# Kernel tuning notes

Hardware: AMD Instinct MI355X
Metric: run time of the kernel (lower is better)

Reference implementation:

```python
import jax, jax.numpy as jnp
import numpy as np

NEG_BIG = -9e15
ALPHA = 0.1  # leaky relu slope


def setup_inputs() -> dict:
    key = jax.random.key(0)
    k1, k2, k3, k4 = jax.random.split(key, 4)
    B, C, N, F = 4, 4, 2048, 64
    x = jax.random.normal(k1, (B, C, N, F), dtype=jnp.float32)
    adj = jax.random.randint(k2, (N, N), 0, 2, dtype=jnp.int32)
    # xavier_uniform on shape (1,1,F,1): fan_in=1, fan_out=F -> bound = 1.414*sqrt(6/(1+F))
    bound = 1.414 * np.sqrt(6.0 / (1.0 + F))
    a1 = jax.random.uniform(k3, (F, 1), jnp.float32, -bound, bound)
    a2 = jax.random.uniform(k4, (F, 1), jnp.float32, -bound, bound)
    return {"x": x, "adj": adj, "a1": a1, "a2": a2}


def reference(x, adj, a1, a2):
    # x: [B, C, N, F]; adj: [N, N]; a1, a2: [F, 1]
    h = x
    f1 = jnp.einsum("bcnf,fo->bcn", h, a1)  # [B, C, N]
    f2 = jnp.einsum("bcnf,fo->bcn", h, a2)  # [B, C, N]
    e = f1[..., :, None] + f2[..., None, :]  # [B, C, N, N] additive scores
    e = jnp.where(e > 0, e, ALPHA * e)       # leaky relu
    e = jnp.where(adj[None, None] > 0, e, jnp.float32(NEG_BIG))
    attention = jax.nn.softmax(e, axis=-1)
    # dropout is identity in eval mode (training=False)
    return jnp.matmul(attention, h)          # [B, C, N, F]
```

## Files before the change

kernel.cpp:

```cpp
#include <hip/hip_runtime.h>
#include <hip/hip_bf16.h>
#include <cstdint>

#define NN 2048
#define FF 64
#define BCC 16

typedef float f32x4 __attribute__((ext_vector_type(4)));
typedef _Float16 half8 __attribute__((ext_vector_type(8)));
typedef uint32_t u32x4 __attribute__((ext_vector_type(4)));


__global__ __launch_bounds__(256) void k_prep(const float* __restrict__ x,
        const int* __restrict__ adj,
        const float* __restrict__ a1, const float* __restrict__ a2,
        _Float16* __restrict__ xP, _Float16* __restrict__ Uh,
        _Float16* __restrict__ Vh, _Float16* __restrict__ CIh,
        unsigned char* __restrict__ ADJP) {
    int wid  = threadIdx.x >> 6;
    int lane = threadIdx.x & 63;

    if (blockIdx.x >= 512) {
        int idx = (blockIdx.x - 512) * 4 + wid;
        int row = idx >> 3, cg = idx & 7;
        const int* p = adj + (size_t)row * NN + cg * 256 + lane;
        unsigned long long m0 = __ballot(p[0]   > 0);
        unsigned long long m1 = __ballot(p[64]  > 0);
        unsigned long long m2 = __ballot(p[128] > 0);
        unsigned long long m3 = __ballot(p[192] > 0);
        if (lane < 32) {
            int q = lane >> 3, s = lane & 7;
            unsigned long long m = (q == 0) ? m0 : (q == 1) ? m1
                                 : (q == 2) ? m2 : m3;
            unsigned char byte = (unsigned char)(m >> (8 * s));
            int jt = (cg * 4 + q) * 2 + (s >> 2);
            int g  = s & 3;
            ADJP[(size_t)row * 256 + g * 64 + jt] = byte;
        }
        return;
    }

    __shared__ float tile[64][65];
    __shared__ float red[2][64][4];
    int bc = blockIdx.x >> 5;
    int n0 = (blockIdx.x & 31) * 64;
    int tx = lane;
    int ty = wid;
    const float* xp = x + ((size_t)bc * NN + n0) * FF;
    #pragma unroll
    for (int k = 0; k < 16; k++) {
        int nl = ty * 16 + k;
        tile[nl][tx] = xp[(size_t)nl * FF + tx];
    }
    __syncthreads();
    int g = lane >> 4, l15 = lane & 15;
    int jt0 = n0 >> 5;
    #pragma unroll
    for (int jl = 0; jl < 2; jl++) {
        half8 val;
        #pragma unroll
        for (int e = 0; e < 8; e++)
            val[e] = (_Float16)tile[jl * 32 + 8 * g + e][ty * 16 + l15];
        ((half8*)xP)[(((size_t)bc * 64 + jt0 + jl) * 4 + ty) * 64 + lane] = val;
    }
    float d1 = 0.f, d2 = 0.f;
    #pragma unroll
    for (int i = 0; i < 16; i++) {
        int f = ty * 16 + i;
        float xv = tile[tx][f];
        d1 += xv * a1[f];
        d2 += xv * a2[f];
    }
    red[0][tx][ty] = d1;
    red[1][tx][ty] = d2;
    __syncthreads();
    if (ty == 0) {
        float f1 = red[0][tx][0] + red[0][tx][1] + red[0][tx][2] + red[0][tx][3];
        float f2 = red[1][tx][0] + red[1][tx][1] + red[1][tx][2] + red[1][tx][3];
        int idx = bc * NN + n0 + tx;
        Uh[idx]  = (_Float16)expf(f2);
        Vh[idx]  = (_Float16)expf(0.1f * f2);
        CIh[idx] = (_Float16)expf(-0.9f * f1);
    }
}

__global__ __launch_bounds__(256) void k_main(
        const _Float16* __restrict__ xP, const _Float16* __restrict__ Uh,
        const _Float16* __restrict__ Vh, const _Float16* __restrict__ CIh,
        const unsigned char* __restrict__ ADJP, float* __restrict__ out) {
    __shared__ _Float16 su[2048];
    __shared__ _Float16 sv[2048];
    __shared__ u32x4 lut[256];
    __shared__ float part[4][16][68];
    __shared__ float zp[4][16];

    int tid = threadIdx.x;
    int jq = tid >> 6, lane = tid & 63;
    int l15 = lane & 15, g = lane >> 4;

    int xcd = blockIdx.x & 7, kk = blockIdx.x >> 3;
    int bc   = (xcd << 1) | (kk >> 5);
    int iblk = kk & 31;
    int i0   = iblk * 64;

    ((u32x4*)su)[tid] = ((const u32x4*)(Uh + bc * NN))[tid];
    ((u32x4*)sv)[tid] = ((const u32x4*)(Vh + bc * NN))[tid];
    {
        uint32_t bb = tid;
        u32x4 lv;
        #pragma unroll
        for (int w = 0; w < 4; w++)
            lv[w] = (((bb >> (2 * w)) & 1u) ? 0xFFFFu : 0u)
                  | (((bb >> (2 * w + 1)) & 1u) ? 0xFFFF0000u : 0u);
        lut[bb] = lv;
    }
    const unsigned char* ab = ADJP + g * 64 + jq * 16;
    u32x4 adjw0 = *(const u32x4*)(ab + (size_t)(i0 + l15) * 256);
    u32x4 adjw1 = *(const u32x4*)(ab + (size_t)(i0 + 16 + l15) * 256);
    u32x4 adjw2 = *(const u32x4*)(ab + (size_t)(i0 + 32 + l15) * 256);
    u32x4 adjw3 = *(const u32x4*)(ab + (size_t)(i0 + 48 + l15) * 256);
    _Float16 Ci0 = CIh[bc * NN + i0 + l15];
    _Float16 Ci1 = CIh[bc * NN + i0 + 16 + l15];
    _Float16 Ci2 = CIh[bc * NN + i0 + 32 + l15];
    _Float16 Ci3 = CIh[bc * NN + i0 + 48 + l15];
    __syncthreads();

    f32x4 acc[4][4];
    #pragma unroll
    for (int a = 0; a < 4; a++)
        #pragma unroll
        for (int nb = 0; nb < 4; nb++)
            acc[a][nb] = (f32x4){0.f, 0.f, 0.f, 0.f};
    f32x4 accz[4];
    #pragma unroll
    for (int a = 0; a < 4; a++) accz[a] = (f32x4){0.f, 0.f, 0.f, 0.f};
    half8 onesh;
    #pragma unroll
    for (int e = 0; e < 8; e++) onesh[e] = (_Float16)1.0f;

    const u32x4* xPbc = (const u32x4*)xP + (size_t)bc * 16384;

    u32x4 A_x0, A_x1, A_x2, A_x3, B_x0, B_x1, B_x2, B_x3;

#define LOADX(P, J) do {                                                      \
        const u32x4* xw_ = xPbc + (((size_t)(jq * 16 + (J))) << 8) + lane;    \
        P##x0 = xw_[0]; P##x1 = xw_[64]; P##x2 = xw_[128]; P##x3 = xw_[192];  \
    } while (0)

#define GEN(AF, ADJW, CI) do {                                                \
        uint32_t b_ = (ADJW[(J_) >> 2] >> (((J_) & 3) * 8)) & 0xffu;          \
        u32x4 mm_ = lut[b_];                                                  \
        half8 mx_ = __builtin_elementwise_max(uu_, vv_ * (CI));               \
        AF = __builtin_bit_cast(half8, __builtin_bit_cast(u32x4, mx_) & mm_); \
    } while (0)

#define COMP(P, J) do {                                                       \
        const int J_ = (J);                                                   \
        const int jo_ = (jq * 16 + J_) * 32 + 8 * g;                          \
        half8 uu_ = *(const half8*)&su[jo_];                                  \
        half8 vv_ = *(const half8*)&sv[jo_];                                  \
        half8 af0_, af1_, af2_, af3_;                                         \
        GEN(af0_, adjw0, Ci0); GEN(af1_, adjw1, Ci1);                         \
        GEN(af2_, adjw2, Ci2); GEN(af3_, adjw3, Ci3);                         \
        half8 b0_ = __builtin_bit_cast(half8, P##x0);                         \
        half8 b1_ = __builtin_bit_cast(half8, P##x1);                         \
        half8 b2_ = __builtin_bit_cast(half8, P##x2);                         \
        half8 b3_ = __builtin_bit_cast(half8, P##x3);                         \
        acc[0][0] = __builtin_amdgcn_mfma_f32_16x16x32_f16(af0_, b0_, acc[0][0], 0, 0, 0); \
        acc[0][1] = __builtin_amdgcn_mfma_f32_16x16x32_f16(af0_, b1_, acc[0][1], 0, 0, 0); \
        acc[0][2] = __builtin_amdgcn_mfma_f32_16x16x32_f16(af0_, b2_, acc[0][2], 0, 0, 0); \
        acc[0][3] = __builtin_amdgcn_mfma_f32_16x16x32_f16(af0_, b3_, acc[0][3], 0, 0, 0); \
        accz[0]   = __builtin_amdgcn_mfma_f32_16x16x32_f16(af0_, onesh, accz[0], 0, 0, 0); \
        acc[1][0] = __builtin_amdgcn_mfma_f32_16x16x32_f16(af1_, b0_, acc[1][0], 0, 0, 0); \
        acc[1][1] = __builtin_amdgcn_mfma_f32_16x16x32_f16(af1_, b1_, acc[1][1], 0, 0, 0); \
        acc[1][2] = __builtin_amdgcn_mfma_f32_16x16x32_f16(af1_, b2_, acc[1][2], 0, 0, 0); \
        acc[1][3] = __builtin_amdgcn_mfma_f32_16x16x32_f16(af1_, b3_, acc[1][3], 0, 0, 0); \
        accz[1]   = __builtin_amdgcn_mfma_f32_16x16x32_f16(af1_, onesh, accz[1], 0, 0, 0); \
        acc[2][0] = __builtin_amdgcn_mfma_f32_16x16x32_f16(af2_, b0_, acc[2][0], 0, 0, 0); \
        acc[2][1] = __builtin_amdgcn_mfma_f32_16x16x32_f16(af2_, b1_, acc[2][1], 0, 0, 0); \
        acc[2][2] = __builtin_amdgcn_mfma_f32_16x16x32_f16(af2_, b2_, acc[2][2], 0, 0, 0); \
        acc[2][3] = __builtin_amdgcn_mfma_f32_16x16x32_f16(af2_, b3_, acc[2][3], 0, 0, 0); \
        accz[2]   = __builtin_amdgcn_mfma_f32_16x16x32_f16(af2_, onesh, accz[2], 0, 0, 0); \
        acc[3][0] = __builtin_amdgcn_mfma_f32_16x16x32_f16(af3_, b0_, acc[3][0], 0, 0, 0); \
        acc[3][1] = __builtin_amdgcn_mfma_f32_16x16x32_f16(af3_, b1_, acc[3][1], 0, 0, 0); \
        acc[3][2] = __builtin_amdgcn_mfma_f32_16x16x32_f16(af3_, b2_, acc[3][2], 0, 0, 0); \
        acc[3][3] = __builtin_amdgcn_mfma_f32_16x16x32_f16(af3_, b3_, acc[3][3], 0, 0, 0); \
        accz[3]   = __builtin_amdgcn_mfma_f32_16x16x32_f16(af3_, onesh, accz[3], 0, 0, 0); \
    } while (0)

    LOADX(A_, 0);
    LOADX(B_, 1);  COMP(A_, 0);
    LOADX(A_, 2);  COMP(B_, 1);
    LOADX(B_, 3);  COMP(A_, 2);
    LOADX(A_, 4);  COMP(B_, 3);
    LOADX(B_, 5);  COMP(A_, 4);
    LOADX(A_, 6);  COMP(B_, 5);
    LOADX(B_, 7);  COMP(A_, 6);
    LOADX(A_, 8);  COMP(B_, 7);
    LOADX(B_, 9);  COMP(A_, 8);
    LOADX(A_, 10); COMP(B_, 9);
    LOADX(B_, 11); COMP(A_, 10);
    LOADX(A_, 12); COMP(B_, 11);
    LOADX(B_, 13); COMP(A_, 12);
    LOADX(A_, 14); COMP(B_, 13);
    LOADX(B_, 15); COMP(A_, 14);
    COMP(B_, 15);
#undef LOADX
#undef GEN
#undef COMP

    float* outp = out + ((size_t)bc * NN + i0) * FF;
    #pragma unroll
    for (int a = 0; a < 4; a++) {
        #pragma unroll
        for (int nb = 0; nb < 4; nb++)
            #pragma unroll
            for (int r = 0; r < 4; r++)
                part[jq][4 * g + r][nb * 16 + l15] = acc[a][nb][r];
        if (l15 == 0) {
            #pragma unroll
            for (int r = 0; r < 4; r++)
                zp[jq][4 * g + r] = accz[a][r];
        }
        __syncthreads();
        #pragma unroll
        for (int rr = 0; rr < 4; rr++) {
            int row = jq * 4 + rr;
            float s = part[0][row][lane] + part[1][row][lane]
                    + part[2][row][lane] + part[3][row][lane];
            float z = zp[0][row] + zp[1][row] + zp[2][row] + zp[3][row];
            outp[(size_t)(16 * a + row) * FF + lane] = s / z;
        }
        __syncthreads();
    }
}

extern "C" void kernel_launch(void* const* d_in, const int* in_sizes, int n_in,
                              void* d_out, int out_size, void* d_ws, size_t ws_size,
                              hipStream_t stream) {
    const float* x  = (const float*)d_in[0];
    const int* adj  = (const int*)d_in[1];
    const float* a1 = (const float*)d_in[2];
    const float* a2 = (const float*)d_in[3];
    float* out = (float*)d_out;

    char* ws = (char*)d_ws;
    _Float16* xP  = (_Float16*)ws;
    _Float16* Uh  = (_Float16*)(ws + 4194304);
    _Float16* Vh  = (_Float16*)(ws + 4259840);
    _Float16* CIh = (_Float16*)(ws + 4325376);
    unsigned char* ADJP = (unsigned char*)(ws + 4390912);

    k_prep<<<512 + 4096, 256, 0, stream>>>(x, adj, a1, a2, xP, Uh, Vh, CIh, ADJP);
    k_main<<<512, 256, 0, stream>>>(xP, Uh, Vh, CIh, ADJP, out);
}
```

Before: 26.36 us.

## Use 512-thread blocks covering 128 rows, sharing U/V staging across two row groups

Result: slower. 26.92 us (+2.1%).

```diff
diff --git a/kernel.cpp b/kernel.cpp
--- a/kernel.cpp
+++ b/kernel.cpp
@@ -84,45 +84,49 @@
     }
 }
 
-__global__ __launch_bounds__(256) void k_main(
+union SmemU {
+    struct { _Float16 su[2048]; _Float16 sv[2048]; u32x4 lut[256]; } s;
+    struct { float part[8][16][68]; float zp[8][16]; } e;
+};
+
+__global__ __launch_bounds__(512, 2) void k_main(
         const _Float16* __restrict__ xP, const _Float16* __restrict__ Uh,
         const _Float16* __restrict__ Vh, const _Float16* __restrict__ CIh,
         const unsigned char* __restrict__ ADJP, float* __restrict__ out) {
-    __shared__ _Float16 su[2048];
-    __shared__ _Float16 sv[2048];
-    __shared__ u32x4 lut[256];
-    __shared__ float part[4][16][68];
-    __shared__ float zp[4][16];
+    __shared__ SmemU sm;
 
     int tid = threadIdx.x;
-    int jq = tid >> 6, lane = tid & 63;
+    int wid = tid >> 6, lane = tid & 63;
+    int ig = wid >> 2, jq = wid & 3;
     int l15 = lane & 15, g = lane >> 4;
 
     int xcd = blockIdx.x & 7, kk = blockIdx.x >> 3;
-    int bc   = (xcd << 1) | (kk >> 5);
-    int iblk = kk & 31;
-    int i0   = iblk * 64;
-
-    ((u32x4*)su)[tid] = ((const u32x4*)(Uh + bc * NN))[tid];
-    ((u32x4*)sv)[tid] = ((const u32x4*)(Vh + bc * NN))[tid];
-    {
+    int bc   = (xcd << 1) | (kk >> 4);
+    int iblk = kk & 15;
+    int i0   = iblk * 128;
+    int rb   = i0 + ig * 64;
+
+    if (tid < 256) {
+        ((u32x4*)sm.s.su)[tid] = ((const u32x4*)(Uh + bc * NN))[tid];
         uint32_t bb = tid;
         u32x4 lv;
         #pragma unroll
         for (int w = 0; w < 4; w++)
             lv[w] = (((bb >> (2 * w)) & 1u) ? 0xFFFFu : 0u)
                   | (((bb >> (2 * w + 1)) & 1u) ? 0xFFFF0000u : 0u);
-        lut[bb] = lv;
+        sm.s.lut[bb] = lv;
+    } else {
+        ((u32x4*)sm.s.sv)[tid - 256] = ((const u32x4*)(Vh + bc * NN))[tid - 256];
     }
     const unsigned char* ab = ADJP + g * 64 + jq * 16;
-    u32x4 adjw0 = *(const u32x4*)(ab + (size_t)(i0 + l15) * 256);
-    u32x4 adjw1 = *(const u32x4*)(ab + (size_t)(i0 + 16 + l15) * 256);
-    u32x4 adjw2 = *(const u32x4*)(ab + (size_t)(i0 + 32 + l15) * 256);
-    u32x4 adjw3 = *(const u32x4*)(ab + (size_t)(i0 + 48 + l15) * 256);
-    _Float16 Ci0 = CIh[bc * NN + i0 + l15];
-    _Float16 Ci1 = CIh[bc * NN + i0 + 16 + l15];
-    _Float16 Ci2 = CIh[bc * NN + i0 + 32 + l15];
-    _Float16 Ci3 = CIh[bc * NN + i0 + 48 + l15];
+    u32x4 adjw0 = *(const u32x4*)(ab + (size_t)(rb + l15) * 256);
+    u32x4 adjw1 = *(const u32x4*)(ab + (size_t)(rb + 16 + l15) * 256);
+    u32x4 adjw2 = *(const u32x4*)(ab + (size_t)(rb + 32 + l15) * 256);
+    u32x4 adjw3 = *(const u32x4*)(ab + (size_t)(rb + 48 + l15) * 256);
+    _Float16 Ci0 = CIh[bc * NN + rb + l15];
+    _Float16 Ci1 = CIh[bc * NN + rb + 16 + l15];
+    _Float16 Ci2 = CIh[bc * NN + rb + 32 + l15];
+    _Float16 Ci3 = CIh[bc * NN + rb + 48 + l15];
     __syncthreads();
 
     f32x4 acc[4][4];
@@ -141,6 +145,7 @@
     const u32x4* xPbc = (const u32x4*)xP + (size_t)bc * 16384;
 
     u32x4 A_x0, A_x1, A_x2, A_x3, B_x0, B_x1, B_x2, B_x3;
+    u32x4 C_x0, C_x1, C_x2, C_x3;
 
 #define LOADX(P, J) do {                                                      \
         const u32x4* xw_ = xPbc + (((size_t)(jq * 16 + (J))) << 8) + lane;    \
@@ -149,7 +154,7 @@
 
 #define GEN(AF, ADJW, CI) do {                                                \
         uint32_t b_ = (ADJW[(J_) >> 2] >> (((J_) & 3) * 8)) & 0xffu;          \
-        u32x4 mm_ = lut[b_];                                                  \
+        u32x4 mm_ = sm.s.lut[b_];                                             \
         half8 mx_ = __builtin_elementwise_max(uu_, vv_ * (CI));               \
         AF = __builtin_bit_cast(half8, __builtin_bit_cast(u32x4, mx_) & mm_); \
     } while (0)
@@ -157,8 +162,8 @@
 #define COMP(P, J) do {                                                       \
         const int J_ = (J);                                                   \
         const int jo_ = (jq * 16 + J_) * 32 + 8 * g;                          \
-        half8 uu_ = *(const half8*)&su[jo_];                                  \
-        half8 vv_ = *(const half8*)&sv[jo_];                                  \
+        half8 uu_ = *(const half8*)&sm.s.su[jo_];                             \
+        half8 vv_ = *(const half8*)&sm.s.sv[jo_];                             \
         half8 af0_, af1_, af2_, af3_;                                         \
         GEN(af0_, adjw0, Ci0); GEN(af1_, adjw1, Ci1);                         \
         GEN(af2_, adjw2, Ci2); GEN(af3_, adjw3, Ci3);                         \
@@ -188,50 +193,53 @@
         accz[3]   = __builtin_amdgcn_mfma_f32_16x16x32_f16(af3_, onesh, accz[3], 0, 0, 0); \
     } while (0)
 
-    LOADX(A_, 0);
-    LOADX(B_, 1);  COMP(A_, 0);
-    LOADX(A_, 2);  COMP(B_, 1);
-    LOADX(B_, 3);  COMP(A_, 2);
-    LOADX(A_, 4);  COMP(B_, 3);
-    LOADX(B_, 5);  COMP(A_, 4);
-    LOADX(A_, 6);  COMP(B_, 5);
-    LOADX(B_, 7);  COMP(A_, 6);
-    LOADX(A_, 8);  COMP(B_, 7);
-    LOADX(B_, 9);  COMP(A_, 8);
-    LOADX(A_, 10); COMP(B_, 9);
-    LOADX(B_, 11); COMP(A_, 10);
-    LOADX(A_, 12); COMP(B_, 11);
-    LOADX(B_, 13); COMP(A_, 12);
-    LOADX(A_, 14); COMP(B_, 13);
-    LOADX(B_, 15); COMP(A_, 14);
-    COMP(B_, 15);
+    LOADX(A_, 0); LOADX(B_, 1); LOADX(C_, 2);
+    COMP(A_, 0);  LOADX(A_, 3);
+    COMP(B_, 1);  LOADX(B_, 4);
+    COMP(C_, 2);  LOADX(C_, 5);
+    COMP(A_, 3);  LOADX(A_, 6);
+    COMP(B_, 4);  LOADX(B_, 7);
+    COMP(C_, 5);  LOADX(C_, 8);
+    COMP(A_, 6);  LOADX(A_, 9);
+    COMP(B_, 7);  LOADX(B_, 10);
+    COMP(C_, 8);  LOADX(C_, 11);
+    COMP(A_, 9);  LOADX(A_, 12);
+    COMP(B_, 10); LOADX(B_, 13);
+    COMP(C_, 11); LOADX(C_, 14);
+    COMP(A_, 12); LOADX(A_, 15);
+    COMP(B_, 13);
+    COMP(C_, 14);
+    COMP(A_, 15);
 #undef LOADX
 #undef GEN
 #undef COMP
 
     float* outp = out + ((size_t)bc * NN + i0) * FF;
+    int igs = wid >> 2;
     #pragma unroll
     for (int a = 0; a < 4; a++) {
+        __syncthreads();
         #pragma unroll
         for (int nb = 0; nb < 4; nb++)
             #pragma unroll
             for (int r = 0; r < 4; r++)
-                part[jq][4 * g + r][nb * 16 + l15] = acc[a][nb][r];
+                sm.e.part[wid][4 * g + r][nb * 16 + l15] = acc[a][nb][r];
         if (l15 == 0) {
             #pragma unroll
             for (int r = 0; r < 4; r++)
-                zp[jq][4 * g + r] = accz[a][r];
+                sm.e.zp[wid][4 * g + r] = accz[a][r];
         }
         __syncthreads();
         #pragma unroll
         for (int rr = 0; rr < 4; rr++) {
-            int row = jq * 4 + rr;
-            float s = part[0][row][lane] + part[1][row][lane]
-                    + part[2][row][lane] + part[3][row][lane];
-            float z = zp[0][row] + zp[1][row] + zp[2][row] + zp[3][row];
-            outp[(size_t)(16 * a + row) * FF + lane] = s / z;
+            int row16 = (wid & 3) * 4 + rr;
+            int base  = igs * 4;
+            float s = sm.e.part[base + 0][row16][lane] + sm.e.part[base + 1][row16][lane]
+                    + sm.e.part[base + 2][row16][lane] + sm.e.part[base + 3][row16][lane];
+            float z = sm.e.zp[base + 0][row16] + sm.e.zp[base + 1][row16]
+                    + sm.e.zp[base + 2][row16] + sm.e.zp[base + 3][row16];
+            outp[(size_t)(igs * 64 + a * 16 + row16) * FF + lane] = s / z;
         }
-        __syncthreads();
     }
 }
 
@@ -252,5 +260,5 @@
     unsigned char* ADJP = (unsigned char*)(ws + 4390912);
 
     k_prep<<<512 + 4096, 256, 0, stream>>>(x, adj, a1, a2, xP, Uh, Vh, CIh, ADJP);
-    k_main<<<512, 256, 0, stream>>>(xP, Uh, Vh, CIh, ADJP, out);
+    k_main<<<256, 512, 0, stream>>>(xP, Uh, Vh, CIh, ADJP, out);
 }
```
